# Kernel tuning notes

Hardware: AMD Instinct MI355X
Metric: run time of the kernel (lower is better)

Reference implementation:

```python
import jax, jax.numpy as jnp
import numpy as np

C = 768
H = 12
N = 257
B = 64
HID = 4 * C
EPS = 1e-5
SCALE = (C // H) ** -0.5


def layer_norm(x, g, b):
    m = x.mean(-1, keepdims=True)
    v = ((x - m) ** 2).mean(-1, keepdims=True)
    return (x - m) * jax.lax.rsqrt(v + EPS) * g + b


def qkv_split(x, qkv_w):
    # x: [B,N,C]; qkv_w: [3C,C] (torch Linear layout)
    qkv = jnp.einsum('bnc,oc->bno', x, qkv_w)  # [B,N,3C]
    qkv = qkv.reshape(x.shape[0], x.shape[1], 3, H, C // H)
    qkv = jnp.transpose(qkv, (2, 0, 3, 1, 4))  # [3,B,H,N,hd]
    return qkv[0], qkv[1], qkv[2]


def self_attn(x, qkv_w, proj_w, proj_b):
    q, k, v = qkv_split(x, qkv_w)
    attn = jax.nn.softmax(jnp.einsum('bhnd,bhmd->bhnm', q, k) * SCALE, axis=-1)
    o = jnp.einsum('bhnm,bhmd->bhnd', attn, v)
    o = jnp.transpose(o, (0, 2, 1, 3)).reshape(x.shape)
    return jnp.einsum('bnc,oc->bno', o, proj_w) + proj_b


def cross_attn(x, y, qkv_w, proj_w, proj_b):
    qx, _, _ = qkv_split(x, qkv_w)
    _, ky, vy = qkv_split(y, qkv_w)
    attn = jax.nn.softmax(jnp.einsum('bhnd,bhmd->bhnm', qx, ky) * SCALE, axis=-1)
    o = jnp.einsum('bhnm,bhmd->bhnd', attn, vy)
    o = jnp.transpose(o, (0, 2, 1, 3)).reshape(x.shape)
    return jnp.einsum('bnc,oc->bno', o, proj_w) + proj_b, attn.sum(1)  # [B,N,N]


def mlp(x, w1, b1, w2, b2):
    h = jax.nn.gelu(jnp.einsum('bnc,hc->bnh', x, w1) + b1, approximate=False)
    return jnp.einsum('bnh,ch->bnc', h, w2) + b2


def arf(x):
    tmp = (jnp.exp(x) - jnp.exp(-x)) / (jnp.exp(x) + jnp.exp(-x - 4.0))
    return jnp.where(tmp < 0, jnp.zeros_like(x), tmp)


def setup_inputs() -> dict:
    key = jax.random.key(0)
    ks = jax.random.split(key, 16)
    s = 0.02
    return {
        'src': jax.random.normal(ks[0], (B, N, C), jnp.float32),
        'tgt': jax.random.normal(ks[1], (B, N, C), jnp.float32),
        'sattn_qkv_w': jax.random.normal(ks[2], (3 * C, C), jnp.float32) * s,
        'sattn_proj_w': jax.random.normal(ks[3], (C, C), jnp.float32) * s,
        'sattn_proj_b': jnp.zeros((C,), jnp.float32),
        'cattn_qkv_w': jax.random.normal(ks[4], (3 * C, C), jnp.float32) * s,
        'cattn_proj_w': jax.random.normal(ks[5], (C, C), jnp.float32) * s,
        'cattn_proj_b': jnp.zeros((C,), jnp.float32),
        'norm1_g': jnp.ones((C,), jnp.float32),
        'norm1_b': jnp.zeros((C,), jnp.float32),
        'norm2_g': jnp.ones((C,), jnp.float32),
        'norm2_b': jnp.zeros((C,), jnp.float32),
        'fc1_w': jax.random.normal(ks[6], (HID, C), jnp.float32) * s,
        'fc1_b': jnp.zeros((HID,), jnp.float32),
        'fc2_w': jax.random.normal(ks[7], (C, HID), jnp.float32) * s,
        'fc2_b': jnp.zeros((C,), jnp.float32),
        'sa_weight': jnp.ones((1, 1, C), jnp.float32),
        'pos_embed': jax.random.normal(ks[8], (1, N, C), jnp.float32) * s,
    }


def reference(src, tgt, sattn_qkv_w, sattn_proj_w, sattn_proj_b,
              cattn_qkv_w, cattn_proj_w, cattn_proj_b,
              norm1_g, norm1_b, norm2_g, norm2_b,
              fc1_w, fc1_b, fc2_w, fc2_b, sa_weight, pos_embed):
    src = src + pos_embed
    srct = self_attn(layer_norm(src, norm1_g, norm1_b), sattn_qkv_w, sattn_proj_w, sattn_proj_b)
    tgtt = self_attn(layer_norm(tgt, norm1_g, norm1_b), sattn_qkv_w, sattn_proj_w, sattn_proj_b)
    src = src + srct
    tgt = tgt + tgtt
    src = src + mlp(layer_norm(srct, norm2_g, norm2_b), fc1_w, fc1_b, fc2_w, fc2_b)
    tgt = tgt + mlp(layer_norm(tgtt, norm2_g, norm2_b), fc1_w, fc1_b, fc2_w, fc2_b)
    srct, attn_src = cross_attn(layer_norm(src, norm1_g, norm1_b),
                                layer_norm(tgt, norm1_g, norm1_b),
                                cattn_qkv_w, cattn_proj_w, cattn_proj_b)
    srct = arf(srct)
    src = src + srct
    src = src + mlp(layer_norm(srct, norm2_g, norm2_b), fc1_w, fc1_b, fc2_w, fc2_b)
    attm_out = attn_src[:, 1:, 1:]
    # heat gate (no grad through attn_src here)
    heat = jax.lax.stop_gradient(attn_src)
    heat = heat.mean(1).reshape(attn_src.shape[0], N, 1)  # [B,N,1]
    gate = jax.nn.sigmoid(heat)
    tgt = tgt + tgt * sa_weight * gate
    return src, tgt, attm_out
```

## Files before the change

### kernel.cpp

```cpp
#include <hip/hip_runtime.h>

#define N_SEQ  257
#define BATCH  64
#define CDIM   768
#define HEADS  12
#define HDIM   64
#define HIDDEN 3072
#define MROWS  (BATCH * N_SEQ)

typedef unsigned short u16;
typedef unsigned int   u32;
typedef __bf16 bf16x8 __attribute__((ext_vector_type(8)));
typedef float  f32x4  __attribute__((ext_vector_type(4)));

__device__ __forceinline__ float b2f(u16 u) { u32 x = ((u32)u) << 16; return __uint_as_float(x); }
__device__ __forceinline__ u16   f2b(float f) {
    u32 x = __float_as_uint(f);
    u32 r = (x + 0x7fffu + ((x >> 16) & 1u)) >> 16;
    return (u16)r;
}
__device__ __forceinline__ float ldf(const float x) { return x; }
__device__ __forceinline__ float ldf(const u16 x)   { return b2f(x); }

__device__ __forceinline__ float geluf(float x) { return 0.5f * x * (1.f + erff(x * 0.70710678118654752f)); }
__device__ __forceinline__ float arff(float x) {
    if (x <= 0.f) return 0.f;
    float a = expf(-2.f * x);
    float c = expf(-2.f * x - 4.f);
    return (1.f - a) / (1.f + c);
}

template<bool MAXOP>
__device__ __forceinline__ float block_red(float v, float* scratch, int tid) {
#pragma unroll
    for (int off = 32; off > 0; off >>= 1) {
        float o = __shfl_down(v, off, 64);
        v = MAXOP ? fmaxf(v, o) : v + o;
    }
    if ((tid & 63) == 0) scratch[tid >> 6] = v;
    __syncthreads();
    float r = MAXOP ? fmaxf(fmaxf(scratch[0], scratch[1]), fmaxf(scratch[2], scratch[3]))
                    : (scratch[0] + scratch[1]) + (scratch[2] + scratch[3]);
    __syncthreads();
    return r;
}

__global__ void detect_kernel(const u16* __restrict__ g1, u32* __restrict__ flag)
{
    if (threadIdx.x == 0 && blockIdx.x == 0) *flag = (g1[0] == 0x3F80u) ? 1u : 0u;
}

__global__ __launch_bounds__(256)
void conv_kernel(const void* __restrict__ s, u16* __restrict__ d, int n,
                 const u32* __restrict__ flag)
{
    const int i = blockIdx.x * 256 + threadIdx.x;
    if (i >= n) return;
    if (*flag) d[i] = ((const u16*)s)[i];
    else       d[i] = f2b(((const float*)s)[i]);
}

#define LDSW 40

template<int EP>
__global__ __launch_bounds__(256)
void gemm_kernel(const u16* __restrict__ A, const u16* __restrict__ W,
                 const u16* __restrict__ bias, u16* __restrict__ Co,
                 float* __restrict__ resid, int M, int Ncols, int K)
{
    __shared__ __align__(16) u16 sA[128 * LDSW];
    __shared__ __align__(16) u16 sB[128 * LDSW];
    const int tid  = threadIdx.x;
    const int bm0  = blockIdx.y * 128;
    const int n0   = blockIdx.x * 128;
    const int lane = tid & 63, wave = tid >> 6;
    const int wm = (wave >> 1) << 6;
    const int wn = (wave & 1) << 6;
    const int r16 = lane & 15, quad = lane >> 4;

    f32x4 acc[4][4] = {};

    for (int k0 = 0; k0 < K; k0 += 32) {
        __syncthreads();
#pragma unroll
        for (int it = 0; it < 2; ++it) {
            int c2  = tid + (it << 8);
            int row = c2 >> 2;
            int col = (c2 & 3) << 3;
            int gm  = bm0 + row; if (gm >= M) gm = M - 1;
            *reinterpret_cast<uint4*>(&sA[row * LDSW + col]) =
                *reinterpret_cast<const uint4*>(A + (size_t)gm * K + k0 + col);
            *reinterpret_cast<uint4*>(&sB[row * LDSW + col]) =
                *reinterpret_cast<const uint4*>(W + (size_t)(n0 + row) * K + k0 + col);
        }
        __syncthreads();

        bf16x8 af[4], bfr[4];
#pragma unroll
        for (int i = 0; i < 4; ++i) {
            af[i]  = *reinterpret_cast<const bf16x8*>(&sA[(wm + i * 16 + r16) * LDSW + quad * 8]);
            bfr[i] = *reinterpret_cast<const bf16x8*>(&sB[(wn + i * 16 + r16) * LDSW + quad * 8]);
        }
#pragma unroll
        for (int i = 0; i < 4; ++i)
#pragma unroll
            for (int j = 0; j < 4; ++j)
                acc[i][j] = __builtin_amdgcn_mfma_f32_16x16x32_bf16(af[i], bfr[j], acc[i][j], 0, 0, 0);
    }

#pragma unroll
    for (int i = 0; i < 4; ++i) {
#pragma unroll
        for (int j = 0; j < 4; ++j) {
            const int gn = n0 + wn + j * 16 + r16;
            const float bv = bias ? b2f(bias[gn]) : 0.f;
#pragma unroll
            for (int r = 0; r < 4; ++r) {
                const int gm = bm0 + wm + i * 16 + quad * 4 + r;
                if (gm < M) {
                    float v = acc[i][j][r] + bv;
                    const size_t oidx = (size_t)gm * Ncols + gn;
                    if (EP == 1) v = geluf(v);
                    if (EP == 3) v = arff(v);
                    if (EP == 0 || EP == 1) Co[oidx] = f2b(v);
                    if (EP == 2 || EP == 3) { Co[oidx] = f2b(v); resid[oidx] += v; }
                    if (EP == 4) resid[oidx] += v;
                }
            }
        }
    }
}

template<typename T>
__global__ __launch_bounds__(256)
void ln_kernel(const T* __restrict__ x, const u16* __restrict__ g,
               const u16* __restrict__ be, u16* __restrict__ y)
{
    __shared__ float scratch[4];
    const int row = blockIdx.x, tid = threadIdx.x;
    const size_t base = (size_t)row * CDIM;
    float v[3];
#pragma unroll
    for (int i = 0; i < 3; ++i) v[i] = ldf(x[base + tid + i * 256]);
    float mean = block_red<false>(v[0] + v[1] + v[2], scratch, tid) * (1.f / 768.f);
    float d0 = v[0] - mean, d1 = v[1] - mean, d2 = v[2] - mean;
    float var = block_red<false>(d0 * d0 + d1 * d1 + d2 * d2, scratch, tid) * (1.f / 768.f);
    float rstd = rsqrtf(var + 1e-5f);
#pragma unroll
    for (int i = 0; i < 3; ++i) {
        int c = tid + i * 256;
        y[base + c] = f2b((v[i] - mean) * rstd * b2f(g[c]) + b2f(be[c]));
    }
}

__global__ __launch_bounds__(256, 2)
void attn_mfma_kernel(const u16* __restrict__ Q, int qs,
                      const u16* __restrict__ Kp, int ks,
                      const u16* __restrict__ Vp, int vs,
                      u16* __restrict__ O, float* __restrict__ asum)
{
    __shared__ __align__(16) u16 Qs[64 * 72];
    __shared__ __align__(16) u16 KP[64 * 72];
    __shared__ __align__(16) u16 Vt[64 * 328];
    const int tid = threadIdx.x;
    const int n0 = blockIdx.x * 64;
    const int h  = blockIdx.y, b = blockIdx.z;
    const int lane = tid & 63, w = tid >> 6;
    const int r16 = lane & 15, quad = lane >> 4;

    {
        int id = tid;
#pragma unroll
        for (int it = 0; it < 2; ++it, id += 256) {
            int row = id >> 3, dc = (id & 7) << 3;
            int gn = n0 + row; if (gn > 256) gn = 256;
            *reinterpret_cast<uint4*>(&Qs[row * 72 + dc]) =
                *reinterpret_cast<const uint4*>(Q + (size_t)(b * N_SEQ + gn) * qs + h * HDIM + dc);
        }
    }
    for (int id = tid; id < 320 * 8; id += 256) {
        int m = id >> 3, dc = (id & 7) << 3;
        int gm = m > 256 ? 256 : m;
        uint4 v4 = *reinterpret_cast<const uint4*>(Vp + (size_t)(b * N_SEQ + gm) * vs + h * HDIM + dc);
        const u16* vv = reinterpret_cast<const u16*>(&v4);
#pragma unroll
        for (int j = 0; j < 8; ++j) Vt[(dc + j) * 328 + m] = vv[j];
    }
    __syncthreads();

    const bf16x8 af0 = *reinterpret_cast<const bf16x8*>(&Qs[(w * 16 + r16) * 72 + quad * 8]);
    const bf16x8 af1 = *reinterpret_cast<const bf16x8*>(&Qs[(w * 16 + r16) * 72 + 32 + quad * 8]);

    f32x4 S[20];
#pragma unroll
    for (int t = 0; t < 20; ++t) S[t] = (f32x4){0.f, 0.f, 0.f, 0.f};

#pragma unroll
    for (int kt = 0; kt < 5; ++kt) {
        __syncthreads();
        int id = tid;
#pragma unroll
        for (int it = 0; it < 2; ++it, id += 256) {
            int row = id >> 3, dc = (id & 7) << 3;
            int gm = kt * 64 + row; if (gm > 256) gm = 256;
            *reinterpret_cast<uint4*>(&KP[row * 72 + dc]) =
                *reinterpret_cast<const uint4*>(Kp + (size_t)(b * N_SEQ + gm) * ks + h * HDIM + dc);
        }
        __syncthreads();
#pragma unroll
        for (int s = 0; s < 4; ++s) {
            bf16x8 b0 = *reinterpret_cast<const bf16x8*>(&KP[(s * 16 + r16) * 72 + quad * 8]);
            bf16x8 b1 = *reinterpret_cast<const bf16x8*>(&KP[(s * 16 + r16) * 72 + 32 + quad * 8]);
            S[kt * 4 + s] = __builtin_amdgcn_mfma_f32_16x16x32_bf16(af0, b0, S[kt * 4 + s], 0, 0, 0);
            S[kt * 4 + s] = __builtin_amdgcn_mfma_f32_16x16x32_bf16(af1, b1, S[kt * 4 + s], 0, 0, 0);
        }
    }
    __syncthreads();

    float inv[4];
#pragma unroll
    for (int r = 0; r < 4; ++r) {
        float m_ = -3.0e38f;
#pragma unroll
        for (int t = 0; t < 20; ++t) {
            int key = t * 16 + r16;
            float v = S[t][r] * 0.125f;
            if (key >= 257) v = -3.0e38f;
            S[t][r] = v;
            m_ = fmaxf(m_, v);
        }
#pragma unroll
        for (int msk = 1; msk < 16; msk <<= 1) m_ = fmaxf(m_, __shfl_xor(m_, msk, 64));
        float s_ = 0.f;
#pragma unroll
        for (int t = 0; t < 20; ++t) {
            float p = __expf(S[t][r] - m_);
            S[t][r] = p; s_ += p;
        }
#pragma unroll
        for (int msk = 1; msk < 16; msk <<= 1) s_ += __shfl_xor(s_, msk, 64);
        inv[r] = 1.f / s_;
    }

    if (asum) {
#pragma unroll
        for (int r = 0; r < 4; ++r) {
            const int n = n0 + w * 16 + quad * 4 + r;
            if (n < N_SEQ) {
#pragma unroll
                for (int t = 0; t < 20; ++t) {
                    int key = t * 16 + r16;
                    if (key < N_SEQ)
                        atomicAdd(&asum[((size_t)b * N_SEQ + n) * N_SEQ + key], S[t][r] * inv[r]);
                }
            }
        }
    }

    f32x4 O4[4];
#pragma unroll
    for (int s = 0; s < 4; ++s) O4[s] = (f32x4){0.f, 0.f, 0.f, 0.f};

#pragma unroll
    for (int kt = 0; kt < 5; ++kt) {
#pragma unroll
        for (int ts = 0; ts < 4; ++ts)
#pragma unroll
            for (int r = 0; r < 4; ++r)
                KP[(w * 16 + quad * 4 + r) * 72 + ts * 16 + r16] = f2b(S[kt * 4 + ts][r]);
        bf16x8 p0 = *reinterpret_cast<const bf16x8*>(&KP[(w * 16 + r16) * 72 + quad * 8]);
        bf16x8 p1 = *reinterpret_cast<const bf16x8*>(&KP[(w * 16 + r16) * 72 + 32 + quad * 8]);
#pragma unroll
        for (int s = 0; s < 4; ++s) {
            bf16x8 v0 = *reinterpret_cast<const bf16x8*>(&Vt[(s * 16 + r16) * 328 + kt * 64 + quad * 8]);
            bf16x8 v1 = *reinterpret_cast<const bf16x8*>(&Vt[(s * 16 + r16) * 328 + kt * 64 + 32 + quad * 8]);
            O4[s] = __builtin_amdgcn_mfma_f32_16x16x32_bf16(p0, v0, O4[s], 0, 0, 0);
            O4[s] = __builtin_amdgcn_mfma_f32_16x16x32_bf16(p1, v1, O4[s], 0, 0, 0);
        }
    }

#pragma unroll
    for (int s = 0; s < 4; ++s) {
#pragma unroll
        for (int r = 0; r < 4; ++r) {
            const int n = n0 + w * 16 + quad * 4 + r;
            if (n < N_SEQ)
                O[(size_t)(b * N_SEQ + n) * CDIM + h * HDIM + s * 16 + r16] = f2b(O4[s][r] * inv[r]);
        }
    }
}

__global__ __launch_bounds__(256)
void init_kernel(const void* __restrict__ src, const void* __restrict__ tgt,
                 const void* __restrict__ pos, float* __restrict__ sa,
                 float* __restrict__ ta, const u32* __restrict__ flag)
{
    const u32 i = blockIdx.x * 256 + threadIdx.x;
    const u32 p = i % (u32)(N_SEQ * CDIM);
    float sv, tv, pv;
    if (*flag) {
        sv = b2f(((const u16*)src)[i]); tv = b2f(((const u16*)tgt)[i]); pv = b2f(((const u16*)pos)[p]);
    } else {
        sv = ((const float*)src)[i];    tv = ((const float*)tgt)[i];    pv = ((const float*)pos)[p];
    }
    sa[i] = sv + pv;
    ta[i] = tv;
}

__global__ __launch_bounds__(256)
void zero_kernel(float* __restrict__ p, int n)
{
    const int i = blockIdx.x * 256 + threadIdx.x;
    if (i < n) p[i] = 0.f;
}

__global__ __launch_bounds__(256)
void gate_kernel(const float* __restrict__ asum, float* __restrict__ gate)
{
    const int b = blockIdx.x;
    for (int m = threadIdx.x; m < N_SEQ; m += 256) {
        float s = 0.f;
        for (int q = 0; q < N_SEQ; ++q)
            s += asum[((size_t)b * N_SEQ + q) * N_SEQ + m];
        s *= (1.f / 257.f);
        gate[b * N_SEQ + m] = 1.f / (1.f + expf(-s));
    }
}

__global__ __launch_bounds__(256)
void final_kernel(const float* __restrict__ sa, const float* __restrict__ ta,
                  const u16* __restrict__ saw, const float* __restrict__ gate,
                  void* __restrict__ osrc_v, const u32* __restrict__ flag)
{
    const u32 i = blockIdx.x * 256 + threadIdx.x;
    const int c  = i % CDIM;
    const int bn = i / CDIM;
    const float so = sa[i];
    const float to = ta[i] * (1.f + b2f(saw[c]) * gate[bn]);
    const size_t BNC = (size_t)MROWS * CDIM;
    if (*flag) {
        u16* o = (u16*)osrc_v;
        o[i] = f2b(so); o[BNC + i] = f2b(to);
    } else {
        float* o = (float*)osrc_v;
        o[i] = so; o[BNC + i] = to;
    }
}

__global__ __launch_bounds__(256)
void attm_kernel(const float* __restrict__ asum, void* __restrict__ out_v,
                 const u32* __restrict__ flag)
{
    const u32 i = blockIdx.x * 256 + threadIdx.x;
    const int b = i >> 16;
    const int r = (i >> 8) & 255;
    const int c = i & 255;
    const float v = asum[((size_t)b * N_SEQ + (r + 1)) * N_SEQ + (c + 1)];
    const size_t off = 2 * (size_t)MROWS * CDIM;
    if (*flag) ((u16*)out_v)[off + i] = f2b(v);
    else       ((float*)out_v)[off + i] = v;
}

extern "C" void kernel_launch(void* const* d_in, const int* in_sizes, int n_in,
                              void* d_out, int out_size, void* d_ws, size_t ws_size,
                              hipStream_t stream)
{
    const void* src    = d_in[0];
    const void* tgt    = d_in[1];
    const void* pos    = d_in[17];

    const int M = MROWS;
    const size_t BNC = (size_t)M * CDIM;

    float* SA   = (float*)d_ws;
    float* TA   = SA + BNC;
    u16*   Cb   = (u16*)(TA + BNC);
    u16*   Db   = Cb + BNC;
    u16*   Eb   = Db + BNC;
    float* ASUM = (float*)(Eb + 4 * BNC);
    float* GATE = ASUM + (size_t)BATCH * N_SEQ * N_SEQ;
    u16*   WB   = (u16*)(GATE + (size_t)BATCH * N_SEQ);
    u16* w_sqkv   = WB;
    u16* w_sproj  = w_sqkv  + 1769472;
    u16* w_sprojb = w_sproj + 589824;
    u16* w_cqkv   = w_sprojb + 768;
    u16* w_cproj  = w_cqkv  + 1769472;
    u16* w_cprojb = w_cproj + 589824;
    u16* w_g1     = w_cprojb + 768;
    u16* w_b1     = w_g1 + 768;
    u16* w_g2     = w_b1 + 768;
    u16* w_b2     = w_g2 + 768;
    u16* w_fc1    = w_b2 + 768;
    u16* w_fc1b   = w_fc1 + 2359296;
    u16* w_fc2    = w_fc1b + 3072;
    u16* w_fc2b   = w_fc2 + 2359296;
    u16* w_saw    = w_fc2b + 768;
    u32* FLAG     = (u32*)(w_saw + 768);
    if (ws_size < (size_t)((char*)(FLAG + 4) - (char*)d_ws)) return;

    const dim3 blk(256, 1, 1);
    const int gM = (M + 127) / 128;
    const dim3 agrid(5, HEADS, BATCH);

    detect_kernel<<<dim3(1), dim3(64), 0, stream>>>((const u16*)d_in[8], FLAG);

    auto conv = [&](int idx, u16* dst, int n) {
        conv_kernel<<<dim3((n + 255) / 256), blk, 0, stream>>>(d_in[idx], dst, n, FLAG);
    };
    conv(2,  w_sqkv,   1769472);
    conv(3,  w_sproj,  589824);
    conv(4,  w_sprojb, 768);
    conv(5,  w_cqkv,   1769472);
    conv(6,  w_cproj,  589824);
    conv(7,  w_cprojb, 768);
    conv(8,  w_g1,     768);
    conv(9,  w_b1,     768);
    conv(10, w_g2,     768);
    conv(11, w_b2,     768);
    conv(12, w_fc1,    2359296);
    conv(13, w_fc1b,   3072);
    conv(14, w_fc2,    2359296);
    conv(15, w_fc2b,   768);
    conv(16, w_saw,    768);

    init_kernel<<<dim3((u32)(BNC / 256)), blk, 0, stream>>>(src, tgt, pos, SA, TA, FLAG);

    ln_kernel<float><<<dim3(M), blk, 0, stream>>>(SA, w_g1, w_b1, Db);
    gemm_kernel<0><<<dim3(2304 / 128, gM), blk, 0, stream>>>(Db, w_sqkv, nullptr, Eb, nullptr, M, 2304, CDIM);
    attn_mfma_kernel<<<agrid, blk, 0, stream>>>(Eb, 2304, Eb + 768, 2304, Eb + 1536, 2304, Db, nullptr);
    gemm_kernel<2><<<dim3(6, gM), blk, 0, stream>>>(Db, w_sproj, w_sprojb, Cb, SA, M, CDIM, CDIM);
    ln_kernel<u16><<<dim3(M), blk, 0, stream>>>(Cb, w_g2, w_b2, Db);
    gemm_kernel<1><<<dim3(HIDDEN / 128, gM), blk, 0, stream>>>(Db, w_fc1, w_fc1b, Eb, nullptr, M, HIDDEN, CDIM);
    gemm_kernel<4><<<dim3(6, gM), blk, 0, stream>>>(Eb, w_fc2, w_fc2b, nullptr, SA, M, CDIM, HIDDEN);

    ln_kernel<float><<<dim3(M), blk, 0, stream>>>(TA, w_g1, w_b1, Db);
    gemm_kernel<0><<<dim3(2304 / 128, gM), blk, 0, stream>>>(Db, w_sqkv, nullptr, Eb, nullptr, M, 2304, CDIM);
    attn_mfma_kernel<<<agrid, blk, 0, stream>>>(Eb, 2304, Eb + 768, 2304, Eb + 1536, 2304, Db, nullptr);
    gemm_kernel<2><<<dim3(6, gM), blk, 0, stream>>>(Db, w_sproj, w_sprojb, Cb, TA, M, CDIM, CDIM);
    ln_kernel<u16><<<dim3(M), blk, 0, stream>>>(Cb, w_g2, w_b2, Db);
    gemm_kernel<1><<<dim3(HIDDEN / 128, gM), blk, 0, stream>>>(Db, w_fc1, w_fc1b, Eb, nullptr, M, HIDDEN, CDIM);
    gemm_kernel<4><<<dim3(6, gM), blk, 0, stream>>>(Eb, w_fc2, w_fc2b, nullptr, TA, M, CDIM, HIDDEN);

    u16* EKV = Eb + BNC;
    ln_kernel<float><<<dim3(M), blk, 0, stream>>>(SA, w_g1, w_b1, Db);
    gemm_kernel<0><<<dim3(6, gM), blk, 0, stream>>>(Db, w_cqkv, nullptr, Eb, nullptr, M, CDIM, CDIM);
    ln_kernel<float><<<dim3(M), blk, 0, stream>>>(TA, w_g1, w_b1, Db);
    gemm_kernel<0><<<dim3(12, gM), blk, 0, stream>>>(Db, w_cqkv + 768 * 768, nullptr, EKV, nullptr, M, 1536, CDIM);
    const int asum_n = BATCH * N_SEQ * N_SEQ;
    zero_kernel<<<dim3((asum_n + 255) / 256), blk, 0, stream>>>(ASUM, asum_n);
    attn_mfma_kernel<<<agrid, blk, 0, stream>>>(Eb, 768, EKV, 1536, EKV + 768, 1536, Db, ASUM);
    gemm_kernel<3><<<dim3(6, gM), blk, 0, stream>>>(Db, w_cproj, w_cprojb, Cb, SA, M, CDIM, CDIM);
    ln_kernel<u16><<<dim3(M), blk, 0, stream>>>(Cb, w_g2, w_b2, Db);
    gemm_kernel<1><<<dim3(HIDDEN / 128, gM), blk, 0, stream>>>(Db, w_fc1, w_fc1b, Eb, nullptr, M, HIDDEN, CDIM);
    gemm_kernel<4><<<dim3(6, gM), blk, 0, stream>>>(Eb, w_fc2, w_fc2b, nullptr, SA, M, CDIM, HIDDEN);

    gate_kernel<<<dim3(BATCH), blk, 0, stream>>>(ASUM, GATE);
    final_kernel<<<dim3((u32)(BNC / 256)), blk, 0, stream>>>(SA, TA, w_saw, GATE, d_out, FLAG);
    attm_kernel<<<dim3(BATCH * 256 * 256 / 256), blk, 0, stream>>>(ASUM, d_out, FLAG);
}
```

Before: 2.680 ms.

## Convert attention to online-softmax flash style to drop the 20-tile score array

Replaces the full 320-key score array held in registers with a per-64-key-tile online softmax (running max, running sum, rescaled output accumulator). This cuts register pressure and may raise occupancy. When the attention sum is requested, a second pass recomputes QK^T to emit normalized probabilities with atomics. The recompute adds extra MFMA and K loads to the cross-attention call, and a separate P buffer raises LDS use.

```diff
diff --git a/kernel.cpp b/kernel.cpp
--- a/kernel.cpp
+++ b/kernel.cpp
@@ -153,14 +153,15 @@
     }
 }
 
-__global__ __launch_bounds__(256, 2)
-void attn_mfma_kernel(const u16* __restrict__ Q, int qs,
-                      const u16* __restrict__ Kp, int ks,
-                      const u16* __restrict__ Vp, int vs,
-                      u16* __restrict__ O, float* __restrict__ asum)
+__global__ __launch_bounds__(256)
+void attn_flash_kernel(const u16* __restrict__ Q, int qs,
+                       const u16* __restrict__ Kp, int ks,
+                       const u16* __restrict__ Vp, int vs,
+                       u16* __restrict__ O, float* __restrict__ asum)
 {
     __shared__ __align__(16) u16 Qs[64 * 72];
-    __shared__ __align__(16) u16 KP[64 * 72];
+    __shared__ __align__(16) u16 Ks[64 * 72];
+    __shared__ __align__(16) u16 Ps[64 * 72];
     __shared__ __align__(16) u16 Vt[64 * 328];
     const int tid = threadIdx.x;
     const int n0 = blockIdx.x * 64;
@@ -191,85 +192,74 @@
     const bf16x8 af0 = *reinterpret_cast<const bf16x8*>(&Qs[(w * 16 + r16) * 72 + quad * 8]);
     const bf16x8 af1 = *reinterpret_cast<const bf16x8*>(&Qs[(w * 16 + r16) * 72 + 32 + quad * 8]);
 
-    f32x4 S[20];
-#pragma unroll
-    for (int t = 0; t < 20; ++t) S[t] = (f32x4){0.f, 0.f, 0.f, 0.f};
-
-#pragma unroll
+    f32x4 O4[4];
+#pragma unroll
+    for (int s = 0; s < 4; ++s) O4[s] = (f32x4){0.f, 0.f, 0.f, 0.f};
+    float m_[4] = { -3.0e38f, -3.0e38f, -3.0e38f, -3.0e38f };
+    float l_[4] = { 0.f, 0.f, 0.f, 0.f };
+
     for (int kt = 0; kt < 5; ++kt) {
         __syncthreads();
-        int id = tid;
-#pragma unroll
-        for (int it = 0; it < 2; ++it, id += 256) {
-            int row = id >> 3, dc = (id & 7) << 3;
-            int gm = kt * 64 + row; if (gm > 256) gm = 256;
-            *reinterpret_cast<uint4*>(&KP[row * 72 + dc]) =
-                *reinterpret_cast<const uint4*>(Kp + (size_t)(b * N_SEQ + gm) * ks + h * HDIM + dc);
+        {
+            int id = tid;
+#pragma unroll
+            for (int it = 0; it < 2; ++it, id += 256) {
+                int row = id >> 3, dc = (id & 7) << 3;
+                int gm = kt * 64 + row; if (gm > 256) gm = 256;
+                *reinterpret_cast<uint4*>(&Ks[row * 72 + dc]) =
+                    *reinterpret_cast<const uint4*>(Kp + (size_t)(b * N_SEQ + gm) * ks + h * HDIM + dc);
+            }
         }
         __syncthreads();
+
+        f32x4 s4[4];
+#pragma unroll
+        for (int s = 0; s < 4; ++s) s4[s] = (f32x4){0.f, 0.f, 0.f, 0.f};
 #pragma unroll
         for (int s = 0; s < 4; ++s) {
-            bf16x8 b0 = *reinterpret_cast<const bf16x8*>(&KP[(s * 16 + r16) * 72 + quad * 8]);
-            bf16x8 b1 = *reinterpret_cast<const bf16x8*>(&KP[(s * 16 + r16) * 72 + 32 + quad * 8]);
-            S[kt * 4 + s] = __builtin_amdgcn_mfma_f32_16x16x32_bf16(af0, b0, S[kt * 4 + s], 0, 0, 0);
-            S[kt * 4 + s] = __builtin_amdgcn_mfma_f32_16x16x32_bf16(af1, b1, S[kt * 4 + s], 0, 0, 0);
-        }
-    }
-    __syncthreads();
-
-    float inv[4];
-#pragma unroll
-    for (int r = 0; r < 4; ++r) {
-        float m_ = -3.0e38f;
-#pragma unroll
-        for (int t = 0; t < 20; ++t) {
-            int key = t * 16 + r16;
-            float v = S[t][r] * 0.125f;
-            if (key >= 257) v = -3.0e38f;
-            S[t][r] = v;
-            m_ = fmaxf(m_, v);
-        }
-#pragma unroll
-        for (int msk = 1; msk < 16; msk <<= 1) m_ = fmaxf(m_, __shfl_xor(m_, msk, 64));
-        float s_ = 0.f;
-#pragma unroll
-        for (int t = 0; t < 20; ++t) {
-            float p = __expf(S[t][r] - m_);
-            S[t][r] = p; s_ += p;
-        }
-#pragma unroll
-        for (int msk = 1; msk < 16; msk <<= 1) s_ += __shfl_xor(s_, msk, 64);
-        inv[r] = 1.f / s_;
-    }
-
-    if (asum) {
+            bf16x8 b0 = *reinterpret_cast<const bf16x8*>(&Ks[(s * 16 + r16) * 72 + quad * 8]);
+            bf16x8 b1 = *reinterpret_cast<const bf16x8*>(&Ks[(s * 16 + r16) * 72 + 32 + quad * 8]);
+            s4[s] = __builtin_amdgcn_mfma_f32_16x16x32_bf16(af0, b0, s4[s], 0, 0, 0);
+            s4[s] = __builtin_amdgcn_mfma_f32_16x16x32_bf16(af1, b1, s4[s], 0, 0, 0);
+        }
+
+#pragma unroll
+        for (int s = 0; s < 4; ++s)
+#pragma unroll
+            for (int r = 0; r < 4; ++r) {
+                float v = s4[s][r] * 0.125f;
+                if (kt == 4 && (s * 16 + r16) >= 1) v = -3.0e38f;
+                s4[s][r] = v;
+            }
+
 #pragma unroll
         for (int r = 0; r < 4; ++r) {
-            const int n = n0 + w * 16 + quad * 4 + r;
-            if (n < N_SEQ) {
-#pragma unroll
-                for (int t = 0; t < 20; ++t) {
-                    int key = t * 16 + r16;
-                    if (key < N_SEQ)
-                        atomicAdd(&asum[((size_t)b * N_SEQ + n) * N_SEQ + key], S[t][r] * inv[r]);
-                }
-            }
-        }
-    }
-
-    f32x4 O4[4];
-#pragma unroll
-    for (int s = 0; s < 4; ++s) O4[s] = (f32x4){0.f, 0.f, 0.f, 0.f};
-
-#pragma unroll
-    for (int kt = 0; kt < 5; ++kt) {
+            float tmax = fmaxf(fmaxf(s4[0][r], s4[1][r]), fmaxf(s4[2][r], s4[3][r]));
+#pragma unroll
+            for (int msk = 1; msk < 16; msk <<= 1) tmax = fmaxf(tmax, __shfl_xor(tmax, msk, 64));
+            float mn = fmaxf(m_[r], tmax);
+            float corr = __expf(m_[r] - mn);
+            m_[r] = mn;
+            float rs = 0.f;
+#pragma unroll
+            for (int s = 0; s < 4; ++s) {
+                float p = __expf(s4[s][r] - mn);
+                s4[s][r] = p; rs += p;
+            }
+#pragma unroll
+            for (int msk = 1; msk < 16; msk <<= 1) rs += __shfl_xor(rs, msk, 64);
+            l_[r] = l_[r] * corr + rs;
+#pragma unroll
+            for (int s = 0; s < 4; ++s) O4[s][r] *= corr;
+        }
+
 #pragma unroll
         for (int ts = 0; ts < 4; ++ts)
 #pragma unroll
             for (int r = 0; r < 4; ++r)
-                KP[(w * 16 + quad * 4 + r) * 72 + ts * 16 + r16] = f2b(S[kt * 4 + ts][r]);
-        bf16x8 p0 = *reinterpret_cast<const bf16x8*>(&KP[(w * 16 + r16) * 72 + quad * 8]);
-        bf16x8 p1 = *reinterpret_cast<const bf16x8*>(&KP[(w * 16 + r16) * 72 + 32 + quad * 8]);
+                Ps[(w * 16 + quad * 4 + r) * 72 + ts * 16 + r16] = f2b(s4[ts][r]);
+        bf16x8 p0 = *reinterpret_cast<const bf16x8*>(&Ps[(w * 16 + r16) * 72 + quad * 8]);
+        bf16x8 p1 = *reinterpret_cast<const bf16x8*>(&Ps[(w * 16 + r16) * 72 + 32 + quad * 8]);
 #pragma unroll
         for (int s = 0; s < 4; ++s) {
             bf16x8 v0 = *reinterpret_cast<const bf16x8*>(&Vt[(s * 16 + r16) * 328 + kt * 64 + quad * 8]);
@@ -279,6 +269,10 @@
         }
     }
 
+    float inv[4];
+#pragma unroll
+    for (int r = 0; r < 4; ++r) inv[r] = 1.f / l_[r];
+
 #pragma unroll
     for (int s = 0; s < 4; ++s) {
 #pragma unroll
@@ -286,6 +280,45 @@
             const int n = n0 + w * 16 + quad * 4 + r;
             if (n < N_SEQ)
                 O[(size_t)(b * N_SEQ + n) * CDIM + h * HDIM + s * 16 + r16] = f2b(O4[s][r] * inv[r]);
+        }
+    }
+
+    if (asum) {
+        for (int kt = 0; kt < 5; ++kt) {
+            __syncthreads();
+            {
+                int id = tid;
+#pragma unroll
+                for (int it = 0; it < 2; ++it, id += 256) {
+                    int row = id >> 3, dc = (id & 7) << 3;
+                    int gm = kt * 64 + row; if (gm > 256) gm = 256;
+                    *reinterpret_cast<uint4*>(&Ks[row * 72 + dc]) =
+                        *reinterpret_cast<const uint4*>(Kp + (size_t)(b * N_SEQ + gm) * ks + h * HDIM + dc);
+                }
+            }
+            __syncthreads();
+
+            f32x4 s4[4];
+#pragma unroll
+            for (int s = 0; s < 4; ++s) s4[s] = (f32x4){0.f, 0.f, 0.f, 0.f};
+#pragma unroll
+            for (int s = 0; s < 4; ++s) {
+                bf16x8 b0 = *reinterpret_cast<const bf16x8*>(&Ks[(s * 16 + r16) * 72 + quad * 8]);
+                bf16x8 b1 = *reinterpret_cast<const bf16x8*>(&Ks[(s * 16 + r16) * 72 + 32 + quad * 8]);
+                s4[s] = __builtin_amdgcn_mfma_f32_16x16x32_bf16(af0, b0, s4[s], 0, 0, 0);
+                s4[s] = __builtin_amdgcn_mfma_f32_16x16x32_bf16(af1, b1, s4[s], 0, 0, 0);
+            }
+#pragma unroll
+            for (int s = 0; s < 4; ++s)
+#pragma unroll
+                for (int r = 0; r < 4; ++r) {
+                    const int key = kt * 64 + s * 16 + r16;
+                    const int n = n0 + w * 16 + quad * 4 + r;
+                    if (key < N_SEQ && n < N_SEQ) {
+                        float p = __expf(s4[s][r] * 0.125f - m_[r]) * inv[r];
+                        atomicAdd(&asum[((size_t)b * N_SEQ + n) * N_SEQ + key], p);
+                    }
+                }
         }
     }
 }
@@ -427,7 +460,7 @@
 
     ln_kernel<float><<<dim3(M), blk, 0, stream>>>(SA, w_g1, w_b1, Db);
     gemm_kernel<0><<<dim3(2304 / 128, gM), blk, 0, stream>>>(Db, w_sqkv, nullptr, Eb, nullptr, M, 2304, CDIM);
-    attn_mfma_kernel<<<agrid, blk, 0, stream>>>(Eb, 2304, Eb + 768, 2304, Eb + 1536, 2304, Db, nullptr);
+    attn_flash_kernel<<<agrid, blk, 0, stream>>>(Eb, 2304, Eb + 768, 2304, Eb + 1536, 2304, Db, nullptr);
     gemm_kernel<2><<<dim3(6, gM), blk, 0, stream>>>(Db, w_sproj, w_sprojb, Cb, SA, M, CDIM, CDIM);
     ln_kernel<u16><<<dim3(M), blk, 0, stream>>>(Cb, w_g2, w_b2, Db);
     gemm_kernel<1><<<dim3(HIDDEN / 128, gM), blk, 0, stream>>>(Db, w_fc1, w_fc1b, Eb, nullptr, M, HIDDEN, CDIM);
@@ -435,7 +468,7 @@
 
     ln_kernel<float><<<dim3(M), blk, 0, stream>>>(TA, w_g1, w_b1, Db);
     gemm_kernel<0><<<dim3(2304 / 128, gM), blk, 0, stream>>>(Db, w_sqkv, nullptr, Eb, nullptr, M, 2304, CDIM);
-    attn_mfma_kernel<<<agrid, blk, 0, stream>>>(Eb, 2304, Eb + 768, 2304, Eb + 1536, 2304, Db, nullptr);
+    attn_flash_kernel<<<agrid, blk, 0, stream>>>(Eb, 2304, Eb + 768, 2304, Eb + 1536, 2304, Db, nullptr);
     gemm_kernel<2><<<dim3(6, gM), blk, 0, stream>>>(Db, w_sproj, w_sprojb, Cb, TA, M, CDIM, CDIM);
     ln_kernel<u16><<<dim3(M), blk, 0, stream>>>(Cb, w_g2, w_b2, Db);
     gemm_kernel<1><<<dim3(HIDDEN / 128, gM), blk, 0, stream>>>(Db, w_fc1, w_fc1b, Eb, nullptr, M, HIDDEN, CDIM);
@@ -448,7 +481,7 @@
     gemm_kernel<0><<<dim3(12, gM), blk, 0, stream>>>(Db, w_cqkv + 768 * 768, nullptr, EKV, nullptr, M, 1536, CDIM);
     const int asum_n = BATCH * N_SEQ * N_SEQ;
     zero_kernel<<<dim3((asum_n + 255) / 256), blk, 0, stream>>>(ASUM, asum_n);
-    attn_mfma_kernel<<<agrid, blk, 0, stream>>>(Eb, 768, EKV, 1536, EKV + 768, 1536, Db, ASUM);
+    attn_flash_kernel<<<agrid, blk, 0, stream>>>(Eb, 768, EKV, 1536, EKV + 768, 1536, Db, ASUM);
     gemm_kernel<3><<<dim3(6, gM), blk, 0, stream>>>(Db, w_cproj, w_cprojb, Cb, SA, M, CDIM, CDIM);
     ln_kernel<u16><<<dim3(M), blk, 0, stream>>>(Cb, w_g2, w_b2, Db);
     gemm_kernel<1><<<dim3(HIDDEN / 128, gM), blk, 0, stream>>>(Db, w_fc1, w_fc1b, Eb, nullptr, M, HIDDEN, CDIM);
```

Result: slower. 2.735 ms (+2.1%).
